# Optimization experiments

Hardware: AMD Instinct MI355X
Metric: run time of the kernel (lower is better)

## Reference

```python
import jax, jax.numpy as jnp
import numpy as np

NUM_HEADS = 4
LN_EPS = 1e-5
NEG_INF = -1e9


def _ln(x, g, b):
    mu = jnp.mean(x, axis=-1, keepdims=True)
    var = jnp.mean(jnp.square(x - mu), axis=-1, keepdims=True)
    return (x - mu) * jax.lax.rsqrt(var + LN_EPS) * g + b


def setup_inputs() -> dict:
    key = jax.random.key(0)
    B, L, D, C, E, T, H, NL, MLP = 1024, 200, 64, 32, 32, 8, 256, 3, 256
    P = D + E            # 96
    KIN = H + 2 * T      # 272
    ks = iter(jax.random.split(key, 64))

    def w(shape, fan_in):
        return jax.random.normal(next(ks), shape, dtype=jnp.float32) / np.sqrt(fan_in)

    inp = {}
    inp['x_u'] = jax.random.normal(next(ks), (B, D), dtype=jnp.float32)
    inp['x_ctx'] = jax.random.normal(next(ks), (B, L, D), dtype=jnp.float32)
    inp['t_ctx'] = jax.random.uniform(next(ks), (B, L), dtype=jnp.float32)
    inp['act_u_idx'] = jax.random.randint(next(ks), (B,), 0, C + 1)
    inp['act_ctx_idx'] = jax.random.randint(next(ks), (B, L), 0, C + 1)
    emb = jax.random.normal(next(ks), (C + 1, E), dtype=jnp.float32)
    inp['emb'] = emb.at[0].set(0.0)  # padding_idx=0
    inp['W_in_self'] = w((P, H), P); inp['b_in_self'] = jnp.zeros((H,), jnp.float32)
    inp['W_in_ctx'] = w((P, H), P); inp['b_in_ctx'] = jnp.zeros((H,), jnp.float32)
    inp['freq'] = jax.random.normal(next(ks), (NL, T), dtype=jnp.float32)
    inp['phase'] = jnp.zeros((NL, T), jnp.float32)
    inp['Wq'] = w((NL, H, H), H)
    inp['Wk'] = w((NL, KIN, H), KIN)
    inp['Wv'] = w((NL, KIN, H), KIN)
    inp['Wres'] = w((NL, H, H), H); inp['bres'] = jnp.zeros((NL, H), jnp.float32)
    inp['Wff1'] = w((NL, H, H), H); inp['bff1'] = jnp.zeros((NL, H), jnp.float32)
    inp['Wff2'] = w((NL, H, H), H); inp['bff2'] = jnp.zeros((NL, H), jnp.float32)
    inp['g1'] = jnp.ones((NL, H), jnp.float32); inp['beta1'] = jnp.zeros((NL, H), jnp.float32)
    inp['g2'] = jnp.ones((NL, H), jnp.float32); inp['beta2'] = jnp.zeros((NL, H), jnp.float32)
    inp['W_ro'] = w((H, MLP), H); inp['b_ro'] = jnp.zeros((MLP,), jnp.float32)
    inp['W_cls'] = w((MLP, C), MLP); inp['b_cls'] = jnp.zeros((C,), jnp.float32)
    inp['W_dt'] = w((MLP, 1), MLP); inp['b_dt'] = jnp.zeros((1,), jnp.float32)
    inp['W_rem'] = w((MLP, 1), MLP); inp['b_rem'] = jnp.zeros((1,), jnp.float32)
    return inp


def reference(x_u, x_ctx, t_ctx, act_u_idx, act_ctx_idx, emb,
              W_in_self, b_in_self, W_in_ctx, b_in_ctx,
              freq, phase, Wq, Wk, Wv, Wres, bres,
              Wff1, bff1, Wff2, bff2, g1, beta1, g2, beta2,
              W_ro, b_ro, W_cls, b_cls, W_dt, b_dt, W_rem, b_rem):
    B, L, _ = x_ctx.shape
    H = W_in_self.shape[1]
    nh = NUM_HEADS
    Dh = H // nh
    scale = np.sqrt(Dh).astype(np.float32)

    mask = act_ctx_idx > 0                                   # (B, L)
    e_u = emb[act_u_idx]                                     # (B, E)
    e_ctx = emb[act_ctx_idx]                                 # (B, L, E)
    xu = jnp.concatenate([x_u, e_u], axis=-1)
    xc = jnp.concatenate([x_ctx, e_ctx], axis=-1)
    h = xu @ W_in_self + b_in_self                           # (B, H)
    ctx = xc @ W_in_ctx + b_in_ctx                           # (B, L, H)

    logt = jnp.log1p(jnp.maximum(t_ctx, 0.0))                # (B, L)
    n_layers = Wq.shape[0]
    for i in range(n_layers):
        z = logt[..., None] * freq[i] + phase[i]             # (B, L, T)
        te = jnp.concatenate([jnp.sin(z), jnp.cos(z)], axis=-1)  # (B, L, 2T)
        kv = jnp.concatenate([ctx, te], axis=-1)             # (B, L, H+2T)
        q = (h @ Wq[i]).reshape(B, nh, Dh)                   # (B, h, d)
        k = (kv @ Wk[i]).reshape(B, L, nh, Dh)               # (B, l, h, d)
        v = (kv @ Wv[i]).reshape(B, L, nh, Dh)
        att_logits = jnp.einsum('bhd,blhd->bhl', q, k) / scale
        att_logits = jnp.where(mask[:, None, :], att_logits, NEG_INF)
        att = jax.nn.softmax(att_logits, axis=-1)            # (B, h, l)
        agg = jnp.einsum('bhl,blhd->bhd', att, v).reshape(B, H)
        z1 = _ln(agg + h @ Wres[i] + bres[i], g1[i], beta1[i])
        ff = jax.nn.relu(z1 @ Wff1[i] + bff1[i]) @ Wff2[i] + bff2[i]
        h = _ln(z1 + ff, g2[i], beta2[i])

    z = jax.nn.relu(h @ W_ro + b_ro)
    logits = z @ W_cls + b_cls
    dt_hat = jax.nn.sigmoid(z @ W_dt + b_dt)
    rem_hat = jax.nn.sigmoid(z @ W_rem + b_rem)
    return (logits, dt_hat, rem_hat)
```

## Files before the change

kernel.cpp:

```cpp
#include <hip/hip_runtime.h>
#include <math.h>

namespace {
constexpr int Bc   = 1024;
constexpr int Lc   = 200;
constexpr int Dc   = 64;
constexpr int Ec   = 32;
constexpr int Pc   = 96;
constexpr int Hc   = 256;
constexpr int Tc   = 8;
constexpr int NLc  = 3;
constexpr int KINc = 272;
constexpr int DHc  = 64;
constexpr int Cc   = 32;
constexpr int QS   = 113;
constexpr int Q4   = 452;
constexpr int QP   = 464;
constexpr int CG   = 112;
constexpr int CGW  = 448;
constexpr int XROWS = Bc * Lc + 8;
constexpr int TEBS  = Bc * Lc + 8;
constexpr float LN_EPS_V = 1e-5f;
constexpr float NEG_BIG  = -1e9f;

typedef __attribute__((ext_vector_type(8))) short bf16x8;
typedef __attribute__((ext_vector_type(4))) float f32x4;

__device__ __forceinline__ unsigned short f2bf(float f) {
    union { float f; unsigned int u; } v; v.f = f;
    unsigned int u = v.u;
    unsigned int r = (u + 0x7fffu + ((u >> 16) & 1u)) >> 16;
    return (unsigned short)r;
}
}

__global__ __launch_bounds__(256) void k_kpv(const float* __restrict__ W_in_ctx,
                                             const float* __restrict__ b_in_ctx,
                                             const float* __restrict__ Wv,
                                             const float* __restrict__ Wk,
                                             float* __restrict__ wvp2,
                                             float* __restrict__ kp) {
    int blk = blockIdx.x;
    int i = blk / QS;
    int j = blk - i * QS;
    int t = threadIdx.x;
    __shared__ float wrow[Hc];
    if (j < 96)        wrow[t] = W_in_ctx[j * Hc + t];
    else if (j == 112) wrow[t] = b_in_ctx[t];
    __syncthreads();
    const float* WvL = Wv + (size_t)i * KINc * Hc;
    const float* WkL = Wk + (size_t)i * KINc * Hc;
    float av, ak;
    if (j >= 96 && j < 112) {
        av = WvL[(256 + (j - 96)) * Hc + t];
        ak = WkL[(256 + (j - 96)) * Hc + t];
    } else {
        av = 0.f; ak = 0.f;
        for (int c = 0; c < Hc; ++c) {
            float w = wrow[c];
            av += w * WvL[c * Hc + t];
            ak += w * WkL[c * Hc + t];
        }
    }
    wvp2[(size_t)blk * Hc + t] = av;
    kp[(size_t)blk * Hc + t]   = ak;
}

__global__ __launch_bounds__(256) void k_wbig2(const float* __restrict__ Wq,
                                               const float* __restrict__ kp,
                                               float* __restrict__ wbig) {
    __shared__ float wq_l[64][65];
    __shared__ float kp_l[113][64];
    int blk = blockIdx.x;
    int i = blk >> 4;
    int rem = blk & 15;
    int h = rem >> 2, et = rem & 3;
    int t = threadIdx.x;
    for (int idx = t; idx < 64 * 64; idx += 256) {
        int e = idx >> 6, d = idx & 63;
        wq_l[e][d] = Wq[(size_t)i * Hc * Hc + (size_t)(et * 64 + e) * Hc + h * 64 + d];
    }
    for (int idx = t; idx < 113 * 64; idx += 256) {
        int r = idx >> 6, d = idx & 63;
        kp_l[r][d] = kp[((size_t)i * QS + r) * Hc + h * 64 + d];
    }
    __syncthreads();
    int e  = t & 63;
    int rq = t >> 6;
    for (int r = rq; r < QS; r += 4) {
        float acc = 0.f;
        #pragma unroll
        for (int d = 0; d < 64; ++d) acc += wq_l[e][d] * kp_l[r][d];
        wbig[((size_t)i * Hc + et * 64 + e) * Q4 + h * QS + r] = 0.125f * acc;
    }
}

__global__ __launch_bounds__(64) void k_frag(const float* __restrict__ wvp2,
                                             const float* __restrict__ Wres,
                                             const float* __restrict__ Wff1,
                                             const float* __restrict__ Wff2,
                                             const float* __restrict__ wbig,
                                             unsigned short* __restrict__ wcatF,
                                             unsigned short* __restrict__ wffF,
                                             unsigned short* __restrict__ wbigF) {
    int blk = blockIdx.x;
    int lane = threadIdx.x;
    unsigned short v[8];
    if (blk < NLc * 352) {
        int i = blk / 352;
        int r = blk - i * 352;
        int kk = r >> 4, ct = r & 15;
        int c = ct * 16 + (lane & 15);
        int kb = kk * 32 + (lane >> 4) * 8;
        #pragma unroll
        for (int j = 0; j < 8; ++j) {
            int k = kb + j;
            float val;
            if (k < 448) {
                int hh = k / 112, jj = k - hh * 112;
                val = ((c >> 6) == hh) ? wvp2[((size_t)i * QS + jj) * Hc + c] : 0.f;
            } else {
                val = Wres[(size_t)i * Hc * Hc + (k - 448) * Hc + c];
            }
            v[j] = f2bf(val);
        }
        *(uint4*)&wcatF[(size_t)blk * 64 * 8 + lane * 8] = *(const uint4*)v;
    } else if (blk < NLc * 352 + NLc * 256) {
        int b2 = blk - NLc * 352;
        int i = b2 / 256;
        int rem = b2 - i * 256;
        int w12 = rem >> 7;
        int r = rem & 127;
        int kk = r >> 4, ct = r & 15;
        int c = ct * 16 + (lane & 15);
        int kb = kk * 32 + (lane >> 4) * 8;
        const float* src = (w12 ? Wff2 : Wff1) + (size_t)i * Hc * Hc;
        #pragma unroll
        for (int j = 0; j < 8; ++j) v[j] = f2bf(src[(size_t)(kb + j) * Hc + c]);
        *(uint4*)&wffF[(size_t)b2 * 64 * 8 + lane * 8] = *(const uint4*)v;
    } else {
        int b3 = blk - NLc * 352 - NLc * 256;
        int i = b3 / 232;
        int r = b3 - i * 232;
        int kk = r / 29, ct = r - kk * 29;
        int c = ct * 16 + (lane & 15);
        int kb = kk * 32 + (lane >> 4) * 8;
        #pragma unroll
        for (int j = 0; j < 8; ++j) {
            float val = (c < Q4) ? wbig[((size_t)i * Hc + kb + j) * Q4 + c] : 0.f;
            v[j] = f2bf(val);
        }
        *(uint4*)&wbigF[(size_t)b3 * 64 * 8 + lane * 8] = *(const uint4*)v;
    }
}

__global__ __launch_bounds__(256) void k_h0(const float* __restrict__ x_u,
                                            const int* __restrict__ act_u,
                                            const float* __restrict__ emb,
                                            const float* __restrict__ W,
                                            const float* __restrict__ bias,
                                            float* __restrict__ h) {
    constexpr int R = 16;
    int b0 = blockIdx.x * R;
    int t = threadIdx.x;
    __shared__ float xu[R * Pc];
    for (int idx = t; idx < R * Pc; idx += 256) {
        int r = idx / Pc, j = idx - r * Pc;
        int b = b0 + r;
        float v;
        if (j < Dc) v = x_u[b * Dc + j];
        else        v = emb[act_u[b] * Ec + (j - Dc)];
        xu[idx] = v;
    }
    __syncthreads();
    float acc[R];
    float bb = bias[t];
    #pragma unroll
    for (int r = 0; r < R; ++r) acc[r] = bb;
    for (int j = 0; j < Pc; ++j) {
        float w = W[j * Hc + t];
        #pragma unroll
        for (int r = 0; r < R; ++r) acc[r] += xu[r * Pc + j] * w;
    }
    #pragma unroll
    for (int r = 0; r < R; ++r) h[(b0 + r) * Hc + t] = acc[r];
}

__global__ __launch_bounds__(256) void k_prepx(const float* __restrict__ x_ctx,
                                               const int* __restrict__ act_ctx,
                                               const float* __restrict__ emb,
                                               unsigned short* __restrict__ xtb,
                                               unsigned short* __restrict__ xtTb) {
    constexpr int ST2 = 116;
    __shared__ __align__(16) unsigned short xsT[96 * ST2];
    int blk = blockIdx.x;
    int b  = blk >> 1;
    int h0 = blk & 1;
    int t = threadIdx.x;
    int wv = t >> 6, lane = t & 63;
    int m = lane & 15, kg = lane >> 4;

    bf16x8 ifrag[2];
    #pragma unroll
    for (int hh = 0; hh < 2; ++hh) {
        unsigned short v[8];
        #pragma unroll
        for (int j8 = 0; j8 < 8; ++j8)
            v[j8] = (kg * 8 + j8 == m + 16 * hh) ? (unsigned short)0x3F80u : (unsigned short)0;
        ifrag[hh] = *(const bf16x8*)v;
    }

    for (int tile = wv; tile < 7; tile += 4) {
        int l = h0 * 112 + tile * 16 + m;
        bool valid = l < Lc;
        bf16x8 afr[3];
        #pragma unroll
        for (int kk = 0; kk < 2; ++kk) {
            unsigned short tmp[8];
            if (valid) {
                const float* s = x_ctx + ((size_t)(b * Lc + l)) * Dc + kk * 32 + kg * 8;
                float4 a0 = *(const float4*)s;
                float4 a1 = *(const float4*)(s + 4);
                tmp[0]=f2bf(a0.x); tmp[1]=f2bf(a0.y); tmp[2]=f2bf(a0.z); tmp[3]=f2bf(a0.w);
                tmp[4]=f2bf(a1.x); tmp[5]=f2bf(a1.y); tmp[6]=f2bf(a1.z); tmp[7]=f2bf(a1.w);
            } else {
                #pragma unroll
                for (int j = 0; j < 8; ++j) tmp[j] = 0;
            }
            afr[kk] = *(const bf16x8*)tmp;
        }
        {
            unsigned short tmp[8];
            if (valid) {
                int a = act_ctx[b * Lc + l];
                const float* s = emb + (size_t)a * Ec + kg * 8;
                float4 e0 = *(const float4*)s;
                float4 e1 = *(const float4*)(s + 4);
                tmp[0]=f2bf(e0.x); tmp[1]=f2bf(e0.y); tmp[2]=f2bf(e0.z); tmp[3]=f2bf(e0.w);
                tmp[4]=f2bf(e1.x); tmp[5]=f2bf(e1.y); tmp[6]=f2bf(e1.z); tmp[7]=f2bf(e1.w);
            } else {
                #pragma unroll
                for (int j = 0; j < 8; ++j) tmp[j] = 0;
            }
            afr[2] = *(const bf16x8*)tmp;
        }
        if (valid) {
            unsigned short* dst = xtb + ((size_t)(b * Lc + l)) * 96;
            *(uint4*)(dst + kg * 8)      = *(const uint4*)&afr[0];
            *(uint4*)(dst + 32 + kg * 8) = *(const uint4*)&afr[1];
            *(uint4*)(dst + 64 + kg * 8) = *(const uint4*)&afr[2];
        }
        #pragma unroll
        for (int kk = 0; kk < 3; ++kk) {
            #pragma unroll
            for (int hh = 0; hh < 2; ++hh) {
                f32x4 d = {0.f, 0.f, 0.f, 0.f};
                d = __builtin_amdgcn_mfma_f32_16x16x32_bf16(afr[kk], ifrag[hh], d, 0, 0, 0);
                int j  = kk * 32 + hh * 16 + m;
                int l0 = tile * 16 + kg * 4;
                unsigned int u0 = (unsigned int)f2bf(d[0]) | ((unsigned int)f2bf(d[1]) << 16);
                unsigned int u1 = (unsigned int)f2bf(d[2]) | ((unsigned int)f2bf(d[3]) << 16);
                uint2 uu; uu.x = u0; uu.y = u1;
                *(uint2*)&xsT[j * ST2 + l0] = uu;
            }
        }
    }
    __syncthreads();

    for (int idx = t; idx < 96 * 14; idx += 256) {
        int j = idx / 14, ch = idx - j * 14;
        uint2 a  = *(const uint2*)&xsT[j * ST2 + ch * 8];
        uint2 b2 = *(const uint2*)&xsT[j * ST2 + ch * 8 + 4];
        uint4 o; o.x = a.x; o.y = a.y; o.z = b2.x; o.w = b2.y;
        *(uint4*)&xtTb[((size_t)(b * 96 + j)) * 224 + h0 * 112 + ch * 8] = o;
    }
}

__global__ __launch_bounds__(256) void k_prept(const float* __restrict__ t_ctx,
                                               const float* __restrict__ freq,
                                               const float* __restrict__ phase,
                                               unsigned short* __restrict__ teb,
                                               unsigned short* __restrict__ teTb) {
    __shared__ float lt[Lc];
    int b = blockIdx.x;
    int t = threadIdx.x;
    if (t < Lc) lt[t] = log1pf(fmaxf(t_ctx[b * Lc + t], 0.f));
    __syncthreads();
    for (int idx = t; idx < NLc * Lc; idx += 256) {
        int i = idx / Lc, l = idx - i * Lc;
        float L = lt[l];
        unsigned short v[16];
        #pragma unroll
        for (int j = 0; j < 8; ++j) {
            float z = L * freq[i * Tc + j] + phase[i * Tc + j];
            v[j]     = f2bf(__sinf(z));
            v[8 + j] = f2bf(__cosf(z));
        }
        size_t base = ((size_t)i * TEBS + b * Lc + l) * 16;
        *(uint4*)&teb[base]     = *(const uint4*)v;
        *(uint4*)&teb[base + 8] = *(const uint4*)&v[8];
    }
    for (int idx = t; idx < NLc * 16 * 28; idx += 256) {
        int i  = idx / 448;
        int r2 = idx - i * 448;
        int f  = r2 / 28, ch = r2 - f * 28;
        int l0 = ch * 8;
        float fr = freq[i * Tc + (f & 7)], ph = phase[i * Tc + (f & 7)];
        bool iscos = f >= 8;
        unsigned short v[8];
        #pragma unroll
        for (int k = 0; k < 8; ++k) {
            int l = l0 + k;
            float val = 0.f;
            if (l < Lc) {
                float z = lt[l] * fr + ph;
                val = iscos ? __cosf(z) : __sinf(z);
            }
            v[k] = f2bf(val);
        }
        *(uint4*)&teTb[((size_t)i * Bc * 16 + b * 16 + f) * 224 + l0] = *(const uint4*)v;
    }
}

__global__ __launch_bounds__(256) void k_qk2b(const float* __restrict__ h,
                                              const float* __restrict__ wbig_l,
                                              unsigned short* __restrict__ qk2b) {
    constexpr int R = 4;
    int rb = blockIdx.x & 255;
    int cb = blockIdx.x >> 8;
    int b0 = rb * R;
    int t = threadIdx.x;
    int c = cb * 256 + t;
    __shared__ float hl[R * Hc];
    for (int idx = t; idx < R * Hc; idx += 256) hl[idx] = h[b0 * Hc + idx];
    __syncthreads();
    if (c >= QP) return;
    if (c >= Q4) {
        #pragma unroll
        for (int r = 0; r < R; ++r) qk2b[(size_t)(b0 + r) * QP + c] = 0;
        return;
    }
    float acc[R];
    #pragma unroll
    for (int r = 0; r < R; ++r) acc[r] = 0.f;
    for (int e = 0; e < Hc; ++e) {
        float w = wbig_l[(size_t)e * Q4 + c];
        #pragma unroll
        for (int r = 0; r < R; ++r) acc[r] += hl[r * Hc + e] * w;
    }
    #pragma unroll
    for (int r = 0; r < R; ++r) qk2b[(size_t)(b0 + r) * QP + c] = f2bf(acc[r]);
}

__global__ __launch_bounds__(256) void k_att(const int* __restrict__ act_ctx,
                                             const unsigned short* __restrict__ qk2b,
                                             const unsigned short* __restrict__ xtb,
                                             const unsigned short* __restrict__ xtTb,
                                             const unsigned short* __restrict__ teb_l,
                                             const unsigned short* __restrict__ teTb_l,
                                             float* __restrict__ cagg) {
    __shared__ unsigned short qks[QP];
    __shared__ float S[4][208];
    __shared__ unsigned short Pl[16][232];
    int b = blockIdx.x;
    int t = threadIdx.x;
    int wv = t >> 6, lane = t & 63;
    int kg = lane >> 4;

    if (t < QP / 2) ((unsigned int*)qks)[t] = ((const unsigned int*)(qk2b + (size_t)b * QP))[t];
    __syncthreads();

    bf16x8 bfr[4];
    {
        int h = lane & 15;
        int kb = kg * 8;
        #pragma unroll
        for (int kk = 0; kk < 4; ++kk) {
            unsigned short tmp[8];
            #pragma unroll
            for (int j = 0; j < 8; ++j) {
                int k = kk * 32 + kb + j;
                tmp[j] = (h < 4 && k < QS) ? qks[h * QS + k] : (unsigned short)0;
            }
            bfr[kk] = *(const bf16x8*)tmp;
        }
    }

    const unsigned short* xrow  = xtb   + (size_t)b * Lc * 96;
    const unsigned short* terow = teb_l + (size_t)b * Lc * 16;
    for (int tile = wv; tile < 13; tile += 4) {
        int r = tile * 16 + (lane & 15);
        bf16x8 a0 = *(const bf16x8*)(xrow + (size_t)r * 96 + kg * 8);
        bf16x8 a1 = *(const bf16x8*)(xrow + (size_t)r * 96 + 32 + kg * 8);
        bf16x8 a2 = *(const bf16x8*)(xrow + (size_t)r * 96 + 64 + kg * 8);
        bf16x8 a3;
        if (kg < 2) {
            a3 = *(const bf16x8*)(terow + (size_t)r * 16 + kg * 8);
        } else if (kg == 2) {
            unsigned short tmp[8] = {0x3F80u, 0, 0, 0, 0, 0, 0, 0};
            a3 = *(const bf16x8*)tmp;
        } else {
            bf16x8 z = {0, 0, 0, 0, 0, 0, 0, 0};
            a3 = z;
        }
        f32x4 acc = {0.f, 0.f, 0.f, 0.f};
        acc = __builtin_amdgcn_mfma_f32_16x16x32_bf16(a0, bfr[0], acc, 0, 0, 0);
        acc = __builtin_amdgcn_mfma_f32_16x16x32_bf16(a1, bfr[1], acc, 0, 0, 0);
        acc = __builtin_amdgcn_mfma_f32_16x16x32_bf16(a2, bfr[2], acc, 0, 0, 0);
        acc = __builtin_amdgcn_mfma_f32_16x16x32_bf16(a3, bfr[3], acc, 0, 0, 0);
        int h = lane & 15;
        if (h < 4) {
            int rb = tile * 16 + kg * 4;
            #pragma unroll
            for (int q = 0; q < 4; ++q) S[h][rb + q] = acc[q];
        }
    }
    for (int idx = t; idx < 16 * 29; idx += 256) {
        int row = idx / 29, c8 = idx - row * 29;
        uint4 z = {0, 0, 0, 0};
        *(uint4*)&Pl[row][c8 * 8] = z;
    }
    __syncthreads();

    {
        int h = wv;
        float lv[4];
        #pragma unroll
        for (int k = 0; k < 4; ++k) {
            int l = lane + 64 * k;
            if (l < Lc) lv[k] = (act_ctx[b * Lc + l] > 0) ? S[h][l] : NEG_BIG;
            else        lv[k] = -INFINITY;
        }
        float m = fmaxf(fmaxf(lv[0], lv[1]), fmaxf(lv[2], lv[3]));
        #pragma unroll
        for (int off = 32; off >= 1; off >>= 1) m = fmaxf(m, __shfl_xor(m, off));
        float p[4];
        float ssum = 0.f;
        #pragma unroll
        for (int k = 0; k < 4; ++k) {
            int l = lane + 64 * k;
            p[k] = (l < Lc) ? __expf(lv[k] - m) : 0.f;
            ssum += p[k];
        }
        #pragma unroll
        for (int off = 32; off >= 1; off >>= 1) ssum += __shfl_xor(ssum, off);
        float sinv = 1.f / ssum;
        #pragma unroll
        for (int k = 0; k < 4; ++k) {
            int l = lane + 64 * k;
            if (l < Lc) Pl[wv][l] = f2bf(p[k] * sinv);
        }
    }
    __syncthreads();

    const unsigned short* xT  = xtTb   + (size_t)b * 96 * 224;
    const unsigned short* teT = teTb_l + (size_t)b * 16 * 224;
    for (int tile = wv; tile < 7; tile += 4) {
        int n = lane & 15;
        const unsigned short* brow = (tile < 6) ? (xT + ((size_t)(tile * 16 + n)) * 224)
                                                : (teT + (size_t)n * 224);
        f32x4 acc = {0.f, 0.f, 0.f, 0.f};
        #pragma unroll
        for (int kk = 0; kk < 7; ++kk) {
            bf16x8 a  = *(const bf16x8*)&Pl[lane & 15][kk * 32 + kg * 8];
            bf16x8 bb = *(const bf16x8*)(brow + kk * 32 + kg * 8);
            acc = __builtin_amdgcn_mfma_f32_16x16x32_bf16(a, bb, acc, 0, 0, 0);
        }
        if (kg == 0) {
            #pragma unroll
            for (int q = 0; q < 4; ++q)
                cagg[(size_t)b * CGW + q * CG + tile * 16 + n] = acc[q];
        }
    }
}

__global__ __launch_bounds__(512) void k_postq(const float* __restrict__ cagg,
                                               float* __restrict__ h,
                                               const float* __restrict__ wvp2L,
                                               const unsigned short* __restrict__ wcatF_l,
                                               const unsigned short* __restrict__ wff1F_l,
                                               const unsigned short* __restrict__ wff2F_l,
                                               const float* __restrict__ bresL,
                                               const float* __restrict__ bff1L,
                                               const float* __restrict__ bff2L,
                                               const float* __restrict__ g1L,
                                               const float* __restrict__ beta1L,
                                               const float* __restrict__ g2L,
                                               const float* __restrict__ beta2L,
                                               const unsigned short* __restrict__ wbigF_next,
                                               unsigned short* __restrict__ qk2b) {
    __shared__ __align__(16) unsigned short Xa[16 * 712];
    __shared__ float z1f[16 * 260];
    __shared__ __align__(16) unsigned short z1n[16 * 264];
    __shared__ __align__(16) unsigned short fb16[16 * 264];
    int r0 = blockIdx.x * 16;
    int t = threadIdx.x;
    int wv = t >> 6, lane = t & 63;
    int n = lane & 15, kg = lane >> 4;

    for (int idx = t; idx < 16 * 704; idx += 512) {
        int r = idx / 704, c = idx - r * 704;
        float v = (c < 448) ? cagg[(size_t)(r0 + r) * CGW + c]
                            : h[(size_t)(r0 + r) * Hc + (c - 448)];
        Xa[r * 712 + c] = f2bf(v);
    }
    __syncthreads();

    {
        f32x4 acc0 = {0.f,0.f,0.f,0.f}, acc1 = {0.f,0.f,0.f,0.f};
        for (int kk = 0; kk < 22; ++kk) {
            bf16x8 a = *(const bf16x8*)&Xa[(lane & 15) * 712 + kk * 32 + kg * 8];
            bf16x8 b0 = *(const bf16x8*)(wcatF_l + (((size_t)kk * 16 + wv * 2) * 64 + lane) * 8);
            bf16x8 b1 = *(const bf16x8*)(wcatF_l + (((size_t)kk * 16 + wv * 2 + 1) * 64 + lane) * 8);
            acc0 = __builtin_amdgcn_mfma_f32_16x16x32_bf16(a, b0, acc0, 0, 0, 0);
            acc1 = __builtin_amdgcn_mfma_f32_16x16x32_bf16(a, b1, acc1, 0, 0, 0);
        }
        int c0 = (wv * 2) * 16 + n, c1 = (wv * 2 + 1) * 16 + n;
        float bi0 = bresL[c0] + wvp2L[112 * Hc + c0];
        float bi1 = bresL[c1] + wvp2L[112 * Hc + c1];
        #pragma unroll
        for (int q = 0; q < 4; ++q) {
            z1f[(kg * 4 + q) * 260 + c0] = acc0[q] + bi0;
            z1f[(kg * 4 + q) * 260 + c1] = acc1[q] + bi1;
        }
    }
    __syncthreads();
    if (wv < 4) {
        int row = wv * 4 + kg;
        float sm = 0.f, sq = 0.f, vals[16];
        #pragma unroll
        for (int s = 0; s < 16; ++s) {
            float v = z1f[row * 260 + n + 16 * s];
            vals[s] = v; sm += v; sq += v * v;
        }
        #pragma unroll
        for (int off = 8; off >= 1; off >>= 1) { sm += __shfl_xor(sm, off); sq += __shfl_xor(sq, off); }
        float mu = sm * (1.f / 256.f);
        float rstd = rsqrtf(sq * (1.f / 256.f) - mu * mu + LN_EPS_V);
        #pragma unroll
        for (int s = 0; s < 16; ++s) {
            int c = n + 16 * s;
            float v = (vals[s] - mu) * rstd * g1L[c] + beta1L[c];
            z1f[row * 260 + c] = v;
            z1n[row * 264 + c] = f2bf(v);
        }
    }
    __syncthreads();
    {
        f32x4 acc0 = {0.f,0.f,0.f,0.f}, acc1 = {0.f,0.f,0.f,0.f};
        for (int kk = 0; kk < 8; ++kk) {
            bf16x8 a = *(const bf16x8*)&z1n[(lane & 15) * 264 + kk * 32 + kg * 8];
            bf16x8 b0 = *(const bf16x8*)(wff1F_l + (((size_t)kk * 16 + wv * 2) * 64 + lane) * 8);
            bf16x8 b1 = *(const bf16x8*)(wff1F_l + (((size_t)kk * 16 + wv * 2 + 1) * 64 + lane) * 8);
            acc0 = __builtin_amdgcn_mfma_f32_16x16x32_bf16(a, b0, acc0, 0, 0, 0);
            acc1 = __builtin_amdgcn_mfma_f32_16x16x32_bf16(a, b1, acc1, 0, 0, 0);
        }
        int c0 = (wv * 2) * 16 + n, c1 = (wv * 2 + 1) * 16 + n;
        float bi0 = bff1L[c0], bi1 = bff1L[c1];
        #pragma unroll
        for (int q = 0; q < 4; ++q) {
            fb16[(kg * 4 + q) * 264 + c0] = f2bf(fmaxf(acc0[q] + bi0, 0.f));
            fb16[(kg * 4 + q) * 264 + c1] = f2bf(fmaxf(acc1[q] + bi1, 0.f));
        }
    }
    __syncthreads();
    {
        f32x4 acc0 = {0.f,0.f,0.f,0.f}, acc1 = {0.f,0.f,0.f,0.f};
        for (int kk = 0; kk < 8; ++kk) {
            bf16x8 a = *(const bf16x8*)&fb16[(lane & 15) * 264 + kk * 32 + kg * 8];
            bf16x8 b0 = *(const bf16x8*)(wff2F_l + (((size_t)kk * 16 + wv * 2) * 64 + lane) * 8);
            bf16x8 b1 = *(const bf16x8*)(wff2F_l + (((size_t)kk * 16 + wv * 2 + 1) * 64 + lane) * 8);
            acc0 = __builtin_amdgcn_mfma_f32_16x16x32_bf16(a, b0, acc0, 0, 0, 0);
            acc1 = __builtin_amdgcn_mfma_f32_16x16x32_bf16(a, b1, acc1, 0, 0, 0);
        }
        int c0 = (wv * 2) * 16 + n, c1 = (wv * 2 + 1) * 16 + n;
        float bi0 = bff2L[c0], bi1 = bff2L[c1];
        #pragma unroll
        for (int q = 0; q < 4; ++q) {
            int row = kg * 4 + q;
            z1f[row * 260 + c0] = acc0[q] + bi0 + z1f[row * 260 + c0];
            z1f[row * 260 + c1] = acc1[q] + bi1 + z1f[row * 260 + c1];
        }
    }
    __syncthreads();
    if (wv < 4) {
        int row = wv * 4 + kg;
        float sm = 0.f, sq = 0.f, vals[16];
        #pragma unroll
        for (int s = 0; s < 16; ++s) {
            float v = z1f[row * 260 + n + 16 * s];
            vals[s] = v; sm += v; sq += v * v;
        }
        #pragma unroll
        for (int off = 8; off >= 1; off >>= 1) { sm += __shfl_xor(sm, off); sq += __shfl_xor(sq, off); }
        float mu = sm * (1.f / 256.f);
        float rstd = rsqrtf(sq * (1.f / 256.f) - mu * mu + LN_EPS_V);
        #pragma unroll
        for (int s = 0; s < 16; ++s) {
            int c = n + 16 * s;
            float v = (vals[s] - mu) * rstd * g2L[c] + beta2L[c];
            h[(size_t)(r0 + row) * Hc + c] = v;
            z1n[row * 264 + c] = f2bf(v);
        }
    }
    __syncthreads();
    if (wbigF_next) {
        for (int ct = wv; ct < 29; ct += 8) {
            f32x4 acc = {0.f, 0.f, 0.f, 0.f};
            for (int kk = 0; kk < 8; ++kk) {
                bf16x8 a = *(const bf16x8*)&z1n[(lane & 15) * 264 + kk * 32 + kg * 8];
                bf16x8 bb = *(const bf16x8*)(wbigF_next + (((size_t)kk * 29 + ct) * 64 + lane) * 8);
                acc = __builtin_amdgcn_mfma_f32_16x16x32_bf16(a, bb, acc, 0, 0, 0);
            }
            #pragma unroll
            for (int q = 0; q < 4; ++q)
                qk2b[(size_t)(r0 + kg * 4 + q) * QP + ct * 16 + n] = f2bf(acc[q]);
        }
    }
}

__global__ __launch_bounds__(256) void k_head(const float* __restrict__ h,
                                              const float* __restrict__ W_ro,
                                              const float* __restrict__ b_ro,
                                              const float* __restrict__ W_cls,
                                              const float* __restrict__ b_cls,
                                              const float* __restrict__ W_dt,
                                              const float* __restrict__ b_dt,
                                              const float* __restrict__ W_rem,
                                              const float* __restrict__ b_rem,
                                              float* __restrict__ out) {
    constexpr int R = 8;
    int b0 = blockIdx.x * R;
    int t = threadIdx.x;
    int wave = t >> 6, lane = t & 63;
    __shared__ float hl[R * Hc], zl[R * Hc];
    __shared__ float wcls[Hc * Cc];
    __shared__ float wdt[Hc], wrem[Hc];
    for (int idx = t; idx < R * Hc; idx += 256) hl[idx] = h[b0 * Hc + idx];
    for (int idx = t; idx < Hc * Cc; idx += 256) wcls[idx] = W_cls[idx];
    wdt[t] = W_dt[t];
    wrem[t] = W_rem[t];
    __syncthreads();
    float acc[R];
    float br = b_ro[t];
    #pragma unroll
    for (int r = 0; r < R; ++r) acc[r] = br;
    for (int d = 0; d < Hc; ++d) {
        float w = W_ro[d * Hc + t];
        #pragma unroll
        for (int r = 0; r < R; ++r) acc[r] += hl[r * Hc + d] * w;
    }
    #pragma unroll
    for (int r = 0; r < R; ++r) zl[r * Hc + t] = fmaxf(acc[r], 0.f);
    __syncthreads();
    {
        int rr = t >> 5;
        int c = t & 31;
        float a = b_cls[c];
        for (int d = 0; d < Hc; ++d) a += zl[rr * Hc + d] * wcls[d * Cc + c];
        out[(size_t)(b0 + rr) * Cc + c] = a;
    }
    for (int rr = wave * 2; rr < wave * 2 + 2; ++rr) {
        float sd = 0.f, sr = 0.f;
        #pragma unroll
        for (int k2 = 0; k2 < 4; ++k2) {
            float zv = zl[rr * Hc + lane + 64 * k2];
            sd += zv * wdt[lane + 64 * k2];
            sr += zv * wrem[lane + 64 * k2];
        }
        #pragma unroll
        for (int off = 32; off >= 1; off >>= 1) { sd += __shfl_xor(sd, off); sr += __shfl_xor(sr, off); }
        if (lane == 0) {
            out[(size_t)Bc * Cc + b0 + rr]      = 1.f / (1.f + __expf(-(sd + b_dt[0])));
            out[(size_t)Bc * Cc + Bc + b0 + rr] = 1.f / (1.f + __expf(-(sr + b_rem[0])));
        }
    }
}

extern "C" void kernel_launch(void* const* d_in, const int* in_sizes, int n_in,
                              void* d_out, int out_size, void* d_ws, size_t ws_size,
                              hipStream_t stream) {
    const float* x_u      = (const float*)d_in[0];
    const float* x_ctx    = (const float*)d_in[1];
    const float* t_ctx    = (const float*)d_in[2];
    const int*   act_u    = (const int*)d_in[3];
    const int*   act_ctx  = (const int*)d_in[4];
    const float* emb      = (const float*)d_in[5];
    const float* W_in_self = (const float*)d_in[6];
    const float* b_in_self = (const float*)d_in[7];
    const float* W_in_ctx  = (const float*)d_in[8];
    const float* b_in_ctx  = (const float*)d_in[9];
    const float* freq  = (const float*)d_in[10];
    const float* phase = (const float*)d_in[11];
    const float* Wq    = (const float*)d_in[12];
    const float* Wk    = (const float*)d_in[13];
    const float* Wv    = (const float*)d_in[14];
    const float* Wres  = (const float*)d_in[15];
    const float* bres  = (const float*)d_in[16];
    const float* Wff1  = (const float*)d_in[17];
    const float* bff1  = (const float*)d_in[18];
    const float* Wff2  = (const float*)d_in[19];
    const float* bff2  = (const float*)d_in[20];
    const float* g1    = (const float*)d_in[21];
    const float* beta1 = (const float*)d_in[22];
    const float* g2    = (const float*)d_in[23];
    const float* beta2 = (const float*)d_in[24];
    const float* W_ro  = (const float*)d_in[25];
    const float* b_ro  = (const float*)d_in[26];
    const float* W_cls = (const float*)d_in[27];
    const float* b_cls = (const float*)d_in[28];
    const float* W_dt  = (const float*)d_in[29];
    const float* b_dt  = (const float*)d_in[30];
    const float* W_rem = (const float*)d_in[31];
    const float* b_rem = (const float*)d_in[32];

    float* ws    = (float*)d_ws;
    float* hbuf  = ws;
    float* wbig  = hbuf  + (size_t)Bc * Hc;
    float* cagg2 = wbig  + (size_t)NLc * Hc * Q4;
    float* wvp2  = cagg2 + (size_t)Bc * CGW;
    float* kp    = wvp2  + (size_t)NLc * QS * Hc;
    unsigned short* xtb   = (unsigned short*)(kp + (size_t)NLc * QS * Hc);
    unsigned short* xtTb  = xtb   + (size_t)XROWS * 96;
    unsigned short* teb   = xtTb  + (size_t)Bc * 96 * 224;
    unsigned short* teTb  = teb   + (size_t)NLc * TEBS * 16;
    unsigned short* qk2b  = teTb  + (size_t)NLc * Bc * 16 * 224;
    unsigned short* wcatF = qk2b  + (size_t)Bc * QP;
    unsigned short* wffF  = wcatF + (size_t)NLc * 352 * 512;
    unsigned short* wbigF = wffF  + (size_t)NLc * 2 * 128 * 512;
    size_t need = ((size_t)Bc * Hc + (size_t)NLc * Hc * Q4
                  + (size_t)Bc * CGW + 2 * (size_t)NLc * QS * Hc) * 4
                + ((size_t)XROWS * 96 + (size_t)Bc * 96 * 224
                  + (size_t)NLc * TEBS * 16 + (size_t)NLc * Bc * 16 * 224
                  + (size_t)Bc * QP
                  + (size_t)NLc * 352 * 512 + (size_t)NLc * 2 * 128 * 512
                  + (size_t)NLc * 232 * 512) * 2;
    if (ws_size < need) return;

    float* out = (float*)d_out;

    k_kpv<<<NLc * QS, 256, 0, stream>>>(W_in_ctx, b_in_ctx, Wv, Wk, wvp2, kp);
    k_wbig2<<<NLc * 16, 256, 0, stream>>>(Wq, kp, wbig);
    k_frag<<<NLc * (352 + 256 + 232), 64, 0, stream>>>(wvp2, Wres, Wff1, Wff2, wbig,
                                                       wcatF, wffF, wbigF);
    k_h0<<<Bc / 16, 256, 0, stream>>>(x_u, act_u, emb, W_in_self, b_in_self, hbuf);
    k_prepx<<<Bc * 2, 256, 0, stream>>>(x_ctx, act_ctx, emb, xtb, xtTb);
    k_prept<<<Bc, 256, 0, stream>>>(t_ctx, freq, phase, teb, teTb);
    k_qk2b<<<512, 256, 0, stream>>>(hbuf, wbig, qk2b);

    for (int i = 0; i < NLc; ++i) {
        k_att<<<Bc, 256, 0, stream>>>(act_ctx, qk2b, xtb, xtTb,
                                      teb + (size_t)i * TEBS * 16,
                                      teTb + (size_t)i * Bc * 16 * 224, cagg2);
        const unsigned short* wbnext = (i < NLc - 1) ? (wbigF + (size_t)(i + 1) * 232 * 512)
                                                     : (const unsigned short*)nullptr;
        k_postq<<<Bc / 16, 512, 0, stream>>>(cagg2, hbuf,
                                             wvp2 + (size_t)i * QS * Hc,
                                             wcatF + (size_t)i * 352 * 512,
                                             wffF + (size_t)(i * 2) * 128 * 512,
                                             wffF + (size_t)(i * 2 + 1) * 128 * 512,
                                             bres + i * Hc, bff1 + i * Hc, bff2 + i * Hc,
                                             g1 + i * Hc, beta1 + i * Hc,
                                             g2 + i * Hc, beta2 + i * Hc,
                                             wbnext, qk2b);
    }
    k_head<<<Bc / 8, 256, 0, stream>>>(hbuf, W_ro, b_ro, W_cls, b_cls,
                                       W_dt, b_dt, W_rem, b_rem, out);
}
```

Baseline: 236.2 us.

## Keep attention scores in registers and drop LDS staging in k_att

```diff
diff --git a/kernel.cpp b/kernel.cpp
--- a/kernel.cpp
+++ b/kernel.cpp
@@ -359,37 +359,30 @@
                                              const unsigned short* __restrict__ teb_l,
                                              const unsigned short* __restrict__ teTb_l,
                                              float* __restrict__ cagg) {
-    __shared__ unsigned short qks[QP];
-    __shared__ float S[4][208];
-    __shared__ unsigned short Pl[16][232];
     int b = blockIdx.x;
     int t = threadIdx.x;
     int wv = t >> 6, lane = t & 63;
-    int kg = lane >> 4;
-
-    if (t < QP / 2) ((unsigned int*)qks)[t] = ((const unsigned int*)(qk2b + (size_t)b * QP))[t];
-    __syncthreads();
-
+    int m = lane & 15, kg = lane >> 4;
+
+    const unsigned short* qrow = qk2b + (size_t)b * QP;
     bf16x8 bfr[4];
-    {
-        int h = lane & 15;
-        int kb = kg * 8;
-        #pragma unroll
-        for (int kk = 0; kk < 4; ++kk) {
-            unsigned short tmp[8];
-            #pragma unroll
-            for (int j = 0; j < 8; ++j) {
-                int k = kk * 32 + kb + j;
-                tmp[j] = (h < 4 && k < QS) ? qks[h * QS + k] : (unsigned short)0;
-            }
-            bfr[kk] = *(const bf16x8*)tmp;
-        }
-    }
-
+    #pragma unroll
+    for (int kk = 0; kk < 4; ++kk) {
+        unsigned short tmp[8];
+        #pragma unroll
+        for (int j = 0; j < 8; ++j) {
+            int k = kk * 32 + kg * 8 + j;
+            tmp[j] = (m < 4 && k < QS) ? qrow[m * QS + k] : (unsigned short)0;
+        }
+        bfr[kk] = *(const bf16x8*)tmp;
+    }
+
+    f32x4 sa[13];
     const unsigned short* xrow  = xtb   + (size_t)b * Lc * 96;
     const unsigned short* terow = teb_l + (size_t)b * Lc * 16;
-    for (int tile = wv; tile < 13; tile += 4) {
-        int r = tile * 16 + (lane & 15);
+    #pragma unroll
+    for (int tile = 0; tile < 13; ++tile) {
+        int r = tile * 16 + m;
         bf16x8 a0 = *(const bf16x8*)(xrow + (size_t)r * 96 + kg * 8);
         bf16x8 a1 = *(const bf16x8*)(xrow + (size_t)r * 96 + 32 + kg * 8);
         bf16x8 a2 = *(const bf16x8*)(xrow + (size_t)r * 96 + 64 + kg * 8);
@@ -408,68 +401,81 @@
         acc = __builtin_amdgcn_mfma_f32_16x16x32_bf16(a1, bfr[1], acc, 0, 0, 0);
         acc = __builtin_amdgcn_mfma_f32_16x16x32_bf16(a2, bfr[2], acc, 0, 0, 0);
         acc = __builtin_amdgcn_mfma_f32_16x16x32_bf16(a3, bfr[3], acc, 0, 0, 0);
-        int h = lane & 15;
-        if (h < 4) {
-            int rb = tile * 16 + kg * 4;
-            #pragma unroll
-            for (int q = 0; q < 4; ++q) S[h][rb + q] = acc[q];
-        }
-    }
-    for (int idx = t; idx < 16 * 29; idx += 256) {
-        int row = idx / 29, c8 = idx - row * 29;
-        uint4 z = {0, 0, 0, 0};
-        *(uint4*)&Pl[row][c8 * 8] = z;
-    }
-    __syncthreads();
-
-    {
-        int h = wv;
-        float lv[4];
-        #pragma unroll
-        for (int k = 0; k < 4; ++k) {
-            int l = lane + 64 * k;
-            if (l < Lc) lv[k] = (act_ctx[b * Lc + l] > 0) ? S[h][l] : NEG_BIG;
-            else        lv[k] = -INFINITY;
-        }
-        float m = fmaxf(fmaxf(lv[0], lv[1]), fmaxf(lv[2], lv[3]));
-        #pragma unroll
-        for (int off = 32; off >= 1; off >>= 1) m = fmaxf(m, __shfl_xor(m, off));
-        float p[4];
-        float ssum = 0.f;
-        #pragma unroll
-        for (int k = 0; k < 4; ++k) {
-            int l = lane + 64 * k;
-            p[k] = (l < Lc) ? __expf(lv[k] - m) : 0.f;
-            ssum += p[k];
-        }
-        #pragma unroll
-        for (int off = 32; off >= 1; off >>= 1) ssum += __shfl_xor(ssum, off);
-        float sinv = 1.f / ssum;
-        #pragma unroll
-        for (int k = 0; k < 4; ++k) {
-            int l = lane + 64 * k;
-            if (l < Lc) Pl[wv][l] = f2bf(p[k] * sinv);
-        }
-    }
-    __syncthreads();
+        sa[tile] = acc;
+    }
+
+    const int* arow = act_ctx + (size_t)b * Lc;
+    float mx = -INFINITY;
+    #pragma unroll
+    for (int tile = 0; tile < 13; ++tile) {
+        #pragma unroll
+        for (int q = 0; q < 4; ++q) {
+            int l = tile * 16 + kg * 4 + q;
+            float sv;
+            if (l < Lc) sv = (arow[l] > 0) ? sa[tile][q] : NEG_BIG;
+            else        sv = -INFINITY;
+            sa[tile][q] = sv;
+            mx = fmaxf(mx, sv);
+        }
+    }
+    mx = fmaxf(mx, __shfl_xor(mx, 16));
+    mx = fmaxf(mx, __shfl_xor(mx, 32));
+    float ss = 0.f;
+    #pragma unroll
+    for (int tile = 0; tile < 13; ++tile) {
+        #pragma unroll
+        for (int q = 0; q < 4; ++q) {
+            int l = tile * 16 + kg * 4 + q;
+            float p = (l < Lc) ? __expf(sa[tile][q] - mx) : 0.f;
+            sa[tile][q] = p;
+            ss += p;
+        }
+    }
+    ss += __shfl_xor(ss, 16);
+    ss += __shfl_xor(ss, 32);
+    float sinv = 1.f / ss;
+    #pragma unroll
+    for (int tile = 0; tile < 13; ++tile) {
+        #pragma unroll
+        for (int q = 0; q < 4; ++q) sa[tile][q] *= sinv;
+    }
+
+    bf16x8 afr[7];
+    bool hi = kg >= 2;
+    int srcbase = m + ((kg & 1) << 5);
+    #pragma unroll
+    for (int kk = 0; kk < 7; ++kk) {
+        unsigned short av[8];
+        #pragma unroll
+        for (int j = 0; j < 8; ++j) {
+            int src = srcbase + ((j >> 2) << 4);
+            float lo = __shfl(sa[2 * kk][j & 3], src);
+            float hv = (kk < 6) ? __shfl(sa[2 * kk + 1][j & 3], src) : 0.f;
+            float v = hi ? hv : lo;
+            av[j] = (m < 4) ? f2bf(v) : (unsigned short)0;
+        }
+        afr[kk] = *(const bf16x8*)av;
+    }
 
     const unsigned short* xT  = xtTb   + (size_t)b * 96 * 224;
     const unsigned short* teT = teTb_l + (size_t)b * 16 * 224;
-    for (int tile = wv; tile < 7; tile += 4) {
-        int n = lane & 15;
-        const unsigned short* brow = (tile < 6) ? (xT + ((size_t)(tile * 16 + n)) * 224)
-                                                : (teT + (size_t)n * 224);
-        f32x4 acc = {0.f, 0.f, 0.f, 0.f};
-        #pragma unroll
-        for (int kk = 0; kk < 7; ++kk) {
-            bf16x8 a  = *(const bf16x8*)&Pl[lane & 15][kk * 32 + kg * 8];
-            bf16x8 bb = *(const bf16x8*)(brow + kk * 32 + kg * 8);
-            acc = __builtin_amdgcn_mfma_f32_16x16x32_bf16(a, bb, acc, 0, 0, 0);
-        }
-        if (kg == 0) {
+    #pragma unroll
+    for (int pv = 0; pv < 2; ++pv) {
+        int tile = wv + pv * 4;
+        if (tile < 7) {
+            const unsigned short* brow = (tile < 6) ? (xT + ((size_t)(tile * 16 + m)) * 224)
+                                                    : (teT + (size_t)m * 224);
+            f32x4 acc = {0.f, 0.f, 0.f, 0.f};
             #pragma unroll
-            for (int q = 0; q < 4; ++q)
-                cagg[(size_t)b * CGW + q * CG + tile * 16 + n] = acc[q];
+            for (int kk = 0; kk < 7; ++kk) {
+                bf16x8 bb = *(const bf16x8*)(brow + kk * 32 + kg * 8);
+                acc = __builtin_amdgcn_mfma_f32_16x16x32_bf16(afr[kk], bb, acc, 0, 0, 0);
+            }
+            if (kg == 0) {
+                #pragma unroll
+                for (int q = 0; q < 4; ++q)
+                    cagg[(size_t)b * CGW + q * CG + tile * 16 + m] = acc[q];
+            }
         }
     }
 }
```

Measured after the change: 283.5 us. +20.0%, slower.
